# Kernel tuning notes

Hardware: AMD Instinct MI355X
Metric: run time of the kernel (lower is better)

Reference implementation:

```python
import jax, jax.numpy as jnp
import numpy as np

B, T, C = 8, 2048, 1024
H, K = 16, 31  # num_heads, kernel_size; head_size = C // H = 64


def setup_inputs() -> dict:
    key = jax.random.key(0)
    ks = jax.random.split(key, 3)
    x = jax.random.normal(ks[0], (B, T, C), dtype=jnp.float32)
    Wk = jax.random.normal(ks[1], (C, 2 * C), dtype=jnp.float32) * 0.02
    bk = jnp.zeros((2 * C,), dtype=jnp.float32)
    Wck = jax.random.normal(ks[2], (C, K * H), dtype=jnp.float32) * 0.02
    bck = jnp.zeros((K * H,), dtype=jnp.float32)
    gamma = jnp.ones((C,), dtype=jnp.float32)
    beta = jnp.zeros((C,), dtype=jnp.float32)
    conv_bias = jnp.zeros((C,), dtype=jnp.float32)
    return {"x": x, "Wk": Wk, "bk": bk, "Wck": Wck, "bck": bck,
            "gamma": gamma, "beta": beta, "conv_bias": conv_bias}


def _layernorm(x, g, b, eps=1e-5):
    mu = jnp.mean(x, axis=-1, keepdims=True)
    var = jnp.mean(jnp.square(x - mu), axis=-1, keepdims=True)
    return (x - mu) * jax.lax.rsqrt(var + eps) * g + b


def reference(x, Wk, bk, Wck, bck, gamma, beta, conv_bias):
    b, t, c = x.shape
    hd = c // H  # head size
    h = _layernorm(x, gamma, beta)
    pre = h @ Wk + bk                      # [B,T,2C]
    a, gte = jnp.split(pre, 2, axis=-1)
    k = a * jax.nn.sigmoid(gte)            # GLU -> [B,T,C]
    w = (k @ Wck + bck).reshape(b, t, H, K)
    w = jax.nn.softmax(w, axis=-1)         # per-token per-head kernel
    pad = K // 2
    kp = jnp.pad(k, ((0, 0), (pad, pad), (0, 0))).reshape(b, t + 2 * pad, H, hd)
    # depthwise dynamic conv: sum over K shifted slices (no im2col blowup)
    out = sum(w[:, :, :, i:i + 1] * kp[:, i:i + t] for i in range(K))  # [B,T,H,hd]
    out = out.reshape(b, t, c) + conv_bias + x  # bias + residual
    return out
```

## Files before the change

kernel.cpp:

```cpp
#include <hip/hip_runtime.h>


typedef __bf16 bf16_t;
typedef __attribute__((ext_vector_type(8))) __bf16 bf16x8;
typedef __attribute__((ext_vector_type(4))) __bf16 bf16x4;
typedef __attribute__((ext_vector_type(4))) float f32x4;

__device__ __forceinline__ void gload_lds16(const void* g, void* l) {
  void* gg = const_cast<void*>(g);
  __builtin_amdgcn_global_load_lds(
      (__attribute__((address_space(1))) unsigned int*)gg,
      (__attribute__((address_space(3))) unsigned int*)l, 16, 0, 0);
}

__global__ __launch_bounds__(256) void prep_wk(const float* __restrict__ Wk,
                                               bf16_t* __restrict__ WT) {
  __shared__ bf16_t T[64][66];
  int c0 = blockIdx.x * 64;
  int k0 = blockIdx.y * 64;
  int tid = threadIdx.x;
#pragma unroll
  for (int p = 0; p < 4; ++p) {
    int idx = p * 256 + tid;
    int r = idx >> 4;
    int q = idx & 15;
    int strip = q >> 3;
    int col4 = (q & 7) * 4;
    const float* src = Wk + (size_t)(k0 + r) * 2048 + strip * 1024 + (c0 >> 1) + col4;
    float4 v = *(const float4*)src;
#pragma unroll
    for (int j = 0; j < 4; ++j) {
      int cl = (col4 + j) * 2 + strip;
      T[cl][r] = (bf16_t)((&v.x)[j]);
    }
  }
  __syncthreads();
  int c = tid >> 2;
  int kk = (tid & 3) * 16;
#pragma unroll
  for (int u = 0; u < 2; ++u) {
    bf16x8 o;
#pragma unroll
    for (int j = 0; j < 8; ++j) o[j] = T[c][kk + u * 8 + j];
    *(bf16x8*)&WT[(size_t)(c0 + c) * 1024 + k0 + kk + u * 8] = o;
  }
}

__global__ __launch_bounds__(256) void prep_wck(const float* __restrict__ Wck,
                                                bf16_t* __restrict__ WT) {
  __shared__ bf16_t T[64][66];
  int n0 = blockIdx.x * 64;
  int k0 = blockIdx.y * 64;
  int tid = threadIdx.x;
#pragma unroll
  for (int p = 0; p < 4; ++p) {
    int idx = p * 256 + tid;
    int r = idx >> 4;
    int q = idx & 15;
    int col = n0 + q * 4;
    float4 v = {0.f, 0.f, 0.f, 0.f};
    if (col < 496) v = *(const float4*)(Wck + (size_t)(k0 + r) * 496 + col);
#pragma unroll
    for (int j = 0; j < 4; ++j) T[q * 4 + j][r] = (bf16_t)((&v.x)[j]);
  }
  __syncthreads();
  int c = tid >> 2;
  int kk = (tid & 3) * 16;
#pragma unroll
  for (int u = 0; u < 2; ++u) {
    bf16x8 o;
#pragma unroll
    for (int j = 0; j < 8; ++j) o[j] = T[c][kk + u * 8 + j];
    *(bf16x8*)&WT[(size_t)(n0 + c) * 1024 + k0 + kk + u * 8] = o;
  }
}

__global__ __launch_bounds__(256) void ln_kernel(const float* __restrict__ x,
                                                 const float* __restrict__ gamma,
                                                 const float* __restrict__ beta,
                                                 bf16_t* __restrict__ h) {
  int row = blockIdx.x;
  int tid = threadIdx.x;
  int lane = tid & 63, wid = tid >> 6;
  const float4* xr = (const float4*)(x + (size_t)row * 1024);
  float4 v = xr[tid];
  __shared__ float red[4];
  __shared__ float bc[2];
  float s = v.x + v.y + v.z + v.w;
#pragma unroll
  for (int off = 32; off > 0; off >>= 1) s += __shfl_down(s, off);
  if (lane == 0) red[wid] = s;
  __syncthreads();
  if (tid == 0) bc[0] = (red[0] + red[1] + red[2] + red[3]) * (1.f / 1024.f);
  __syncthreads();
  float mu = bc[0];
  float dx = v.x - mu, dy = v.y - mu, dz = v.z - mu, dw = v.w - mu;
  float s2 = dx * dx + dy * dy + dz * dz + dw * dw;
#pragma unroll
  for (int off = 32; off > 0; off >>= 1) s2 += __shfl_down(s2, off);
  if (lane == 0) red[wid] = s2;
  __syncthreads();
  if (tid == 0)
    bc[1] = rsqrtf((red[0] + red[1] + red[2] + red[3]) * (1.f / 1024.f) + 1e-5f);
  __syncthreads();
  float rs = bc[1];
  const float4* g4 = (const float4*)gamma;
  const float4* b4 = (const float4*)beta;
  float4 gv = g4[tid], bv = b4[tid];
  bf16x4 o;
  o[0] = (bf16_t)(dx * rs * gv.x + bv.x);
  o[1] = (bf16_t)(dy * rs * gv.y + bv.y);
  o[2] = (bf16_t)(dz * rs * gv.z + bv.z);
  o[3] = (bf16_t)(dw * rs * gv.w + bv.w);
  *(bf16x4*)&h[(size_t)row * 1024 + tid * 4] = o;
}

__global__ __launch_bounds__(512, 2) void gemm256_glu(const bf16_t* __restrict__ Ag,
                                                      const bf16_t* __restrict__ Bg,
                                                      const float* __restrict__ bias,
                                                      bf16_t* __restrict__ outp) {
  extern __shared__ char smem[];
  const int tid = threadIdx.x;
  const int lane = tid & 63;
  const int wid = tid >> 6;
  const int wr = wid >> 2;
  const int wc = wid & 3;

  int bid = blockIdx.x;
  int swz = (bid & 7) * 64 + (bid >> 3);
  int m0 = (swz >> 3) * 256;
  int n0 = (swz & 7) * 256;

  const int xr = (lane & 7) << 4;
  const int cs0 = (((lane >> 4) << 4) ^ xr);
  const int cs1 = cs0 ^ 64;
  const int aBase = wr * 16384 + (lane & 15) * 128;
  const int bBase = 65536 + (wc >> 1) * 16384 + (wc & 1) * 8192 + (lane & 15) * 128;

  const int sidx0 = tid, sidx1 = tid + 512;
  const int srow0 = sidx0 >> 3, srow1 = sidx1 >> 3;
  const int scol0 = ((((sidx0 & 7) << 4) ^ ((srow0 & 7) << 4)) >> 1);
  const int scol1 = ((((sidx1 & 7) << 4) ^ ((srow1 & 7) << 4)) >> 1);
  const int d0 = sidx0 * 16, d1 = sidx1 * 16;

  f32x4 acc[8][4] = {};
  bf16x8 bq[4][2], pc[2][2], pn[2][2];

#define STAGE_A(buf, h_, kt)                                                          \
  {                                                                                   \
    gload_lds16(Ag + (size_t)(m0 + (h_)*128 + srow0) * 1024 + (kt) + scol0,           \
                smem + (buf)*32768 + (h_)*16384 + d0);                                \
    gload_lds16(Ag + (size_t)(m0 + (h_)*128 + srow1) * 1024 + (kt) + scol1,           \
                smem + (buf)*32768 + (h_)*16384 + d1);                                \
  }
#define STAGE_B(buf, h_, kt)                                                          \
  {                                                                                   \
    gload_lds16(Bg + (size_t)(n0 + (h_)*128 + srow0) * 1024 + (kt) + scol0,           \
                smem + 65536 + (buf)*32768 + (h_)*16384 + d0);                        \
    gload_lds16(Bg + (size_t)(n0 + (h_)*128 + srow1) * 1024 + (kt) + scol1,           \
                smem + 65536 + (buf)*32768 + (h_)*16384 + d1);                        \
  }
#define LDA(buf, f, s) (*(const bf16x8*)(smem + (buf)*32768 + aBase + (f)*2048 + ((s) ? cs1 : cs0)))
#define LDB(buf, g, s) (*(const bf16x8*)(smem + bBase + (buf)*32768 + (g)*2048 + ((s) ? cs1 : cs0)))
#define MFMA_(a, b, c) __builtin_amdgcn_mfma_f32_16x16x32_bf16(a, b, c, 0, 0, 0)
#define RD_PAIR(D, buf, f)                                                            \
  { D[0][0] = LDA(buf, f, 0); D[0][1] = LDA(buf, f, 1);                               \
    D[1][0] = LDA(buf, (f) + 1, 0); D[1][1] = LDA(buf, (f) + 1, 1); }
#define RD_BQ(buf)                                                                    \
  { _Pragma("unroll") for (int g = 0; g < 4; ++g) {                                   \
      bq[g][0] = LDB(buf, g, 0); bq[g][1] = LDB(buf, g, 1); } }
#define MM_PAIR(F0, P)                                                                \
  { _Pragma("unroll") for (int g = 0; g < 4; ++g) {                                   \
      acc[F0][g]       = MFMA_(P[0][0], bq[g][0], acc[F0][g]);                        \
      acc[(F0) + 1][g] = MFMA_(P[1][0], bq[g][0], acc[(F0) + 1][g]);                  \
      acc[F0][g]       = MFMA_(P[0][1], bq[g][1], acc[F0][g]);                        \
      acc[(F0) + 1][g] = MFMA_(P[1][1], bq[g][1], acc[(F0) + 1][g]); } }
#define LGKM0                                                                         \
  asm volatile("s_waitcnt lgkmcnt(0)" ::: "memory");                                  \
  __builtin_amdgcn_sched_barrier(0)
#define BAR __builtin_amdgcn_s_barrier()
#define PRIO1 __builtin_amdgcn_s_setprio(1)
#define PRIO0 __builtin_amdgcn_s_setprio(0)

#define TILE(BUF, NBUF, T)                                                            \
  {                                                                                   \
                                                                              \
    BAR;                                                                              \
    if ((T) < 15) { STAGE_A(NBUF, 0, ((T) + 1) * 64); STAGE_A(NBUF, 1, ((T) + 1) * 64); } \
    LGKM0; PRIO1; MM_PAIR(0, pc); PRIO0;                                              \
    RD_PAIR(pn, BUF, 2);                                                              \
                                                                              \
    BAR;                                                                              \
    LGKM0; PRIO1; MM_PAIR(2, pn); PRIO0;                                              \
    RD_PAIR(pc, BUF, 4);                                                              \
                                                                              \
    BAR;                                                                              \
    if ((T) < 14) STAGE_B(BUF, 0, ((T) + 2) * 64);                                    \
    LGKM0; PRIO1; MM_PAIR(4, pc); PRIO0;                                              \
    RD_PAIR(pn, BUF, 6);                                                              \
                                                                              \
    if ((T) < 14)       { asm volatile("s_waitcnt vmcnt(2)" ::: "memory"); }          \
    else if ((T) == 14) { asm volatile("s_waitcnt vmcnt(0)" ::: "memory"); }          \
    BAR;                                                                              \
    if ((T) < 14) STAGE_B(BUF, 1, ((T) + 2) * 64);                                    \
    LGKM0; PRIO1; MM_PAIR(6, pn); PRIO0;                                              \
    if ((T) < 15) { RD_BQ(NBUF); RD_PAIR(pc, NBUF, 0); }                              \
  }

  STAGE_B(0, 0, 0); STAGE_B(0, 1, 0); STAGE_A(0, 0, 0); STAGE_A(0, 1, 0);
  STAGE_B(1, 0, 64); STAGE_B(1, 1, 64);
  asm volatile("s_waitcnt vmcnt(4)" ::: "memory");
  BAR;
  RD_BQ(0); RD_PAIR(pc, 0, 0);

  for (int t = 0; t < 14; t += 2) {
    TILE(0, 1, t);
    TILE(1, 0, t + 1);
  }
  TILE(0, 1, 14);
  TILE(1, 0, 15);

#pragma unroll
  for (int f = 0; f < 8; ++f) {
    int row = m0 + wr * 128 + f * 16 + ((lane >> 4) << 2);
#pragma unroll
    for (int g = 0; g < 4; ++g) {
      int col = n0 + wc * 64 + g * 16 + (lane & 15);
      int src = (col & 1) ? 1024 + (col >> 1) : (col >> 1);
      float bv = bias[src];
#pragma unroll
      for (int j = 0; j < 4; ++j) {
        float v = acc[f][g][j] + bv;
        float gt = __shfl_xor(v, 1);
        if (!(col & 1)) {
          float kv = v / (1.f + __expf(-gt));
          outp[(size_t)(row + j) * 1024 + (col >> 1)] = (bf16_t)kv;
        }
      }
    }
  }
#undef STAGE_A
#undef STAGE_B
#undef LDA
#undef LDB
#undef MFMA_
#undef RD_PAIR
#undef RD_BQ
#undef MM_PAIR
#undef LGKM0
#undef BAR
#undef PRIO1
#undef PRIO0
#undef TILE
}

__global__ __launch_bounds__(256, 2) void gemm128_bias(const bf16_t* __restrict__ Ag,
                                                       const bf16_t* __restrict__ Bg,
                                                       const float* __restrict__ bias,
                                                       float* __restrict__ outp) {
  __shared__ bf16_t As[2][128 * 32];
  __shared__ bf16_t Bs[2][128 * 32];
  int tid = threadIdx.x;
  int lane = tid & 63;
  int wid = tid >> 6;
  int wr = wid >> 1, wc = wid & 1;
  int n0 = blockIdx.x * 128;
  int m0 = blockIdx.y * 128;

  f32x4 acc[4][4] = {};

#define STAGE(bufi, kt)                                                         \
  {                                                                             \
    _Pragma("unroll") for (int s_ = 0; s_ < 2; ++s_) {                          \
      int idx = (tid + s_ * 256) * 8;                                           \
      int row = idx >> 5;                                                       \
      int col = idx & 31;                                                       \
      gload_lds16(Ag + (size_t)(m0 + row) * 1024 + (kt) + col, &As[bufi][idx]); \
      gload_lds16(Bg + (size_t)(n0 + row) * 1024 + (kt) + col, &Bs[bufi][idx]); \
    }                                                                           \
  }

#define COMPUTE(bufi)                                                           \
  {                                                                             \
    int ko = (lane >> 4) * 8;                                                   \
    int rl = lane & 15;                                                         \
    bf16x8 af[4], bb[4];                                                        \
    _Pragma("unroll") for (int m_ = 0; m_ < 4; ++m_)                            \
        af[m_] = *(const bf16x8*)&As[bufi][(wr * 64 + m_ * 16 + rl) * 32 + ko]; \
    _Pragma("unroll") for (int n_ = 0; n_ < 4; ++n_)                            \
        bb[n_] = *(const bf16x8*)&Bs[bufi][(wc * 64 + n_ * 16 + rl) * 32 + ko]; \
    _Pragma("unroll") for (int m_ = 0; m_ < 4; ++m_)                            \
        _Pragma("unroll") for (int n_ = 0; n_ < 4; ++n_)                        \
            acc[m_][n_] = __builtin_amdgcn_mfma_f32_16x16x32_bf16(              \
                af[m_], bb[n_], acc[m_][n_], 0, 0, 0);                          \
  }

  STAGE(0, 0);
  __syncthreads();
  int buf = 0;
  for (int kt = 32; kt < 1024; kt += 32) {
    STAGE(buf ^ 1, kt);
    COMPUTE(buf);
    __syncthreads();
    buf ^= 1;
  }
  COMPUTE(buf);

#pragma unroll
  for (int m_ = 0; m_ < 4; ++m_) {
    int row = m0 + wr * 64 + m_ * 16 + ((lane >> 4) << 2);
#pragma unroll
    for (int n_ = 0; n_ < 4; ++n_) {
      int col = n0 + wc * 64 + n_ * 16 + (lane & 15);
      float bv = (col < 496) ? bias[col] : 0.f;
#pragma unroll
      for (int j = 0; j < 4; ++j)
        outp[(size_t)(row + j) * 512 + col] = acc[m_][n_][j] + bv;
    }
  }
#undef STAGE
#undef COMPUTE
}

__global__ __launch_bounds__(256) void conv_kernel(const bf16_t* __restrict__ Kin,
                                                   const float* __restrict__ logits,
                                                   const float* __restrict__ x,
                                                   const float* __restrict__ conv_bias,
                                                   float* __restrict__ out) {
  __shared__ bf16_t ks[94][64];
  __shared__ float wls[64][32];
  int tid = threadIdx.x;
  int t0 = blockIdx.x * 64;
  int hh = blockIdx.y;
  int b = blockIdx.z;

  for (int i = tid; i < 94 * 8; i += 256) {
    int r = i >> 3;
    int seg = (i & 7) * 8;
    int t = t0 - 15 + r;
    bf16x8 v = {};
    if (t >= 0 && t < 2048)
      v = *(const bf16x8*)&Kin[((size_t)b * 2048 + t) * 1024 + hh * 64 + seg];
    *(bf16x8*)&ks[r][seg] = v;
  }
  if (tid < 64) {
    int t = t0 + tid;
    const float* lp = logits + ((size_t)b * 2048 + t) * 512 + hh * 31;
    float l[31];
    float mx = -1e30f;
#pragma unroll
    for (int i = 0; i < 31; ++i) { l[i] = lp[i]; mx = fmaxf(mx, l[i]); }
    float ssum = 0.f;
#pragma unroll
    for (int i = 0; i < 31; ++i) { l[i] = __expf(l[i] - mx); ssum += l[i]; }
    float inv = 1.f / ssum;
#pragma unroll
    for (int i = 0; i < 31; ++i) wls[tid][i] = l[i] * inv;
  }
  __syncthreads();

  int lane = tid & 63;
  int tq = tid >> 6;
  float win[46];
#pragma unroll
  for (int j = 0; j < 46; ++j) win[j] = (float)ks[tq * 16 + j][lane];
  float cb = conv_bias[hh * 64 + lane];
#pragma unroll
  for (int j = 0; j < 16; ++j) {
    int trow = tq * 16 + j;
    float wv[31];
#pragma unroll
    for (int i4 = 0; i4 < 7; ++i4) {
      f32x4 w4 = *(const f32x4*)&wls[trow][i4 * 4];
      wv[i4 * 4 + 0] = w4[0]; wv[i4 * 4 + 1] = w4[1];
      wv[i4 * 4 + 2] = w4[2]; wv[i4 * 4 + 3] = w4[3];
    }
    wv[28] = wls[trow][28]; wv[29] = wls[trow][29]; wv[30] = wls[trow][30];
    float a = 0.f;
#pragma unroll
    for (int i = 0; i < 31; ++i) a += wv[i] * win[j + i];
    size_t off = ((size_t)b * 2048 + t0 + trow) * 1024 + hh * 64 + lane;
    out[off] = a + cb + x[off];
  }
}

extern "C" void kernel_launch(void* const* d_in, const int* in_sizes, int n_in,
                              void* d_out, int out_size, void* d_ws, size_t ws_size,
                              hipStream_t stream) {
  const float* x         = (const float*)d_in[0];
  const float* Wk        = (const float*)d_in[1];
  const float* bk        = (const float*)d_in[2];
  const float* Wck       = (const float*)d_in[3];
  const float* bck       = (const float*)d_in[4];
  const float* gamma     = (const float*)d_in[5];
  const float* beta      = (const float*)d_in[6];
  const float* conv_bias = (const float*)d_in[7];
  float* out = (float*)d_out;

  char* ws = (char*)d_ws;
  bf16_t* h      = (bf16_t*)(ws);
  bf16_t* kbuf   = (bf16_t*)(ws + (33554432));
  bf16_t* WT1    = (bf16_t*)(ws + (67108864));
  bf16_t* WT2    = (bf16_t*)(ws + (71303168));
  float*  logits = (float*)(ws + (72351744));

  hipFuncSetAttribute((const void*)gemm256_glu,
                      hipFuncAttributeMaxDynamicSharedMemorySize, 131072);

  prep_wk<<<dim3(32, 16), 256, 0, stream>>>(Wk, WT1);
  prep_wck<<<dim3(8, 16), 256, 0, stream>>>(Wck, WT2);
  ln_kernel<<<16384, 256, 0, stream>>>(x, gamma, beta, h);
  gemm256_glu<<<512, 512, 131072, stream>>>(h, WT1, bk, kbuf);
  gemm128_bias<<<dim3(4, 128), 256, 0, stream>>>(kbuf, WT2, bck, logits);
  conv_kernel<<<dim3(32, 16, 8), 256, 0, stream>>>(kbuf, logits, x, conv_bias, out);
}
```

Before: 290.6 us.

## Fuse softmax into logits GEMM epilogue with head-padded layout, bf16 weights

Reorders the Wck columns so each head occupies 32 slots (31 taps plus one pad), which lets the second GEMM compute the per-head softmax in its epilogue through lane shuffles and store normalized weights as bf16. The conv kernel then reads the precomputed weights with vector loads instead of 64 threads doing a serial 31-wide softmax from fp32 logits. LayerNorm now handles one row per wavefront with shuffle-only reductions and no block barriers. The fused epilogue adds shuffle and exp work to the GEMM, and storing the weights in bf16 lowers their precision.

```diff
diff --git a/kernel.cpp b/kernel.cpp
--- a/kernel.cpp
+++ b/kernel.cpp
@@ -57,11 +57,15 @@
     int idx = p * 256 + tid;
     int r = idx >> 4;
     int q = idx & 15;
-    int col = n0 + q * 4;
-    float4 v = {0.f, 0.f, 0.f, 0.f};
-    if (col < 496) v = *(const float4*)(Wck + (size_t)(k0 + r) * 496 + col);
-#pragma unroll
-    for (int j = 0; j < 4; ++j) T[q * 4 + j][r] = (bf16_t)((&v.x)[j]);
+#pragma unroll
+    for (int j = 0; j < 4; ++j) {
+      int nl = q * 4 + j;
+      int n = n0 + nl;
+      int hh = n >> 5, kk = n & 31;
+      float val = 0.f;
+      if (kk < 31) val = Wck[(size_t)(k0 + r) * 496 + hh * 31 + kk];
+      T[nl][r] = (bf16_t)val;
+    }
   }
   __syncthreads();
   int c = tid >> 2;
@@ -79,40 +83,39 @@
                                                  const float* __restrict__ gamma,
                                                  const float* __restrict__ beta,
                                                  bf16_t* __restrict__ h) {
-  int row = blockIdx.x;
   int tid = threadIdx.x;
-  int lane = tid & 63, wid = tid >> 6;
-  const float4* xr = (const float4*)(x + (size_t)row * 1024);
-  float4 v = xr[tid];
-  __shared__ float red[4];
-  __shared__ float bc[2];
-  float s = v.x + v.y + v.z + v.w;
-#pragma unroll
-  for (int off = 32; off > 0; off >>= 1) s += __shfl_down(s, off);
-  if (lane == 0) red[wid] = s;
-  __syncthreads();
-  if (tid == 0) bc[0] = (red[0] + red[1] + red[2] + red[3]) * (1.f / 1024.f);
-  __syncthreads();
-  float mu = bc[0];
-  float dx = v.x - mu, dy = v.y - mu, dz = v.z - mu, dw = v.w - mu;
-  float s2 = dx * dx + dy * dy + dz * dz + dw * dw;
-#pragma unroll
-  for (int off = 32; off > 0; off >>= 1) s2 += __shfl_down(s2, off);
-  if (lane == 0) red[wid] = s2;
-  __syncthreads();
-  if (tid == 0)
-    bc[1] = rsqrtf((red[0] + red[1] + red[2] + red[3]) * (1.f / 1024.f) + 1e-5f);
-  __syncthreads();
-  float rs = bc[1];
-  const float4* g4 = (const float4*)gamma;
-  const float4* b4 = (const float4*)beta;
-  float4 gv = g4[tid], bv = b4[tid];
-  bf16x4 o;
-  o[0] = (bf16_t)(dx * rs * gv.x + bv.x);
-  o[1] = (bf16_t)(dy * rs * gv.y + bv.y);
-  o[2] = (bf16_t)(dz * rs * gv.z + bv.z);
-  o[3] = (bf16_t)(dw * rs * gv.w + bv.w);
-  *(bf16x4*)&h[(size_t)row * 1024 + tid * 4] = o;
+  int lane = tid & 63;
+  int row = blockIdx.x * 4 + (tid >> 6);
+  const float* xr = x + (size_t)row * 1024;
+  float4 v[4];
+#pragma unroll
+  for (int u = 0; u < 4; ++u) v[u] = *(const float4*)(xr + u * 256 + lane * 4);
+  float s = 0.f;
+#pragma unroll
+  for (int u = 0; u < 4; ++u) s += v[u].x + v[u].y + v[u].z + v[u].w;
+#pragma unroll
+  for (int off = 32; off > 0; off >>= 1) s += __shfl_xor(s, off);
+  float mu = s * (1.f / 1024.f);
+  float s2 = 0.f;
+#pragma unroll
+  for (int u = 0; u < 4; ++u) {
+    float a = v[u].x - mu, b = v[u].y - mu, c = v[u].z - mu, d = v[u].w - mu;
+    s2 += a * a + b * b + c * c + d * d;
+  }
+#pragma unroll
+  for (int off = 32; off > 0; off >>= 1) s2 += __shfl_xor(s2, off);
+  float rs = rsqrtf(s2 * (1.f / 1024.f) + 1e-5f);
+#pragma unroll
+  for (int u = 0; u < 4; ++u) {
+    float4 gv = *(const float4*)(gamma + u * 256 + lane * 4);
+    float4 bv = *(const float4*)(beta + u * 256 + lane * 4);
+    bf16x4 o;
+    o[0] = (bf16_t)((v[u].x - mu) * rs * gv.x + bv.x);
+    o[1] = (bf16_t)((v[u].y - mu) * rs * gv.y + bv.y);
+    o[2] = (bf16_t)((v[u].z - mu) * rs * gv.z + bv.z);
+    o[3] = (bf16_t)((v[u].w - mu) * rs * gv.w + bv.w);
+    *(bf16x4*)&h[(size_t)row * 1024 + u * 256 + lane * 4] = o;
+  }
 }
 
 __global__ __launch_bounds__(512, 2) void gemm256_glu(const bf16_t* __restrict__ Ag,
@@ -254,10 +257,10 @@
 #undef TILE
 }
 
-__global__ __launch_bounds__(256, 2) void gemm128_bias(const bf16_t* __restrict__ Ag,
-                                                       const bf16_t* __restrict__ Bg,
-                                                       const float* __restrict__ bias,
-                                                       float* __restrict__ outp) {
+__global__ __launch_bounds__(256, 2) void gemm128_sm(const bf16_t* __restrict__ Ag,
+                                                     const bf16_t* __restrict__ Bg,
+                                                     const float* __restrict__ bck,
+                                                     bf16_t* __restrict__ Wout) {
   __shared__ bf16_t As[2][128 * 32];
   __shared__ bf16_t Bs[2][128 * 32];
   int tid = threadIdx.x;
@@ -306,16 +309,37 @@
   }
   COMPUTE(buf);
 
+  int s = lane & 15;
+  int slotB = s + 16;
 #pragma unroll
   for (int m_ = 0; m_ < 4; ++m_) {
     int row = m0 + wr * 64 + m_ * 16 + ((lane >> 4) << 2);
 #pragma unroll
-    for (int n_ = 0; n_ < 4; ++n_) {
-      int col = n0 + wc * 64 + n_ * 16 + (lane & 15);
-      float bv = (col < 496) ? bias[col] : 0.f;
-#pragma unroll
-      for (int j = 0; j < 4; ++j)
-        outp[(size_t)(row + j) * 512 + col] = acc[m_][n_][j] + bv;
+    for (int pp = 0; pp < 2; ++pp) {
+      int colA = n0 + wc * 64 + pp * 32 + s;
+      int hh = colA >> 5;
+      float bvA = bck[hh * 31 + s];
+      float bvB = (slotB < 31) ? bck[hh * 31 + slotB] : 0.f;
+#pragma unroll
+      for (int j = 0; j < 4; ++j) {
+        float v0 = acc[m_][2 * pp][j] + bvA;
+        float v1 = (slotB < 31) ? (acc[m_][2 * pp + 1][j] + bvB) : -1e30f;
+        float mx = fmaxf(v0, v1);
+        mx = fmaxf(mx, __shfl_xor(mx, 1));
+        mx = fmaxf(mx, __shfl_xor(mx, 2));
+        mx = fmaxf(mx, __shfl_xor(mx, 4));
+        mx = fmaxf(mx, __shfl_xor(mx, 8));
+        float e0 = __expf(v0 - mx);
+        float e1 = (slotB < 31) ? __expf(v1 - mx) : 0.f;
+        float ss = e0 + e1;
+        ss += __shfl_xor(ss, 1);
+        ss += __shfl_xor(ss, 2);
+        ss += __shfl_xor(ss, 4);
+        ss += __shfl_xor(ss, 8);
+        float inv = 1.f / ss;
+        Wout[(size_t)(row + j) * 512 + colA] = (bf16_t)(e0 * inv);
+        Wout[(size_t)(row + j) * 512 + colA + 16] = (bf16_t)(e1 * inv);
+      }
     }
   }
 #undef STAGE
@@ -323,7 +347,7 @@
 }
 
 __global__ __launch_bounds__(256) void conv_kernel(const bf16_t* __restrict__ Kin,
-                                                   const float* __restrict__ logits,
+                                                   const bf16_t* __restrict__ Wq,
                                                    const float* __restrict__ x,
                                                    const float* __restrict__ conv_bias,
                                                    float* __restrict__ out) {
@@ -343,19 +367,11 @@
       v = *(const bf16x8*)&Kin[((size_t)b * 2048 + t) * 1024 + hh * 64 + seg];
     *(bf16x8*)&ks[r][seg] = v;
   }
-  if (tid < 64) {
-    int t = t0 + tid;
-    const float* lp = logits + ((size_t)b * 2048 + t) * 512 + hh * 31;
-    float l[31];
-    float mx = -1e30f;
-#pragma unroll
-    for (int i = 0; i < 31; ++i) { l[i] = lp[i]; mx = fmaxf(mx, l[i]); }
-    float ssum = 0.f;
-#pragma unroll
-    for (int i = 0; i < 31; ++i) { l[i] = __expf(l[i] - mx); ssum += l[i]; }
-    float inv = 1.f / ssum;
-#pragma unroll
-    for (int i = 0; i < 31; ++i) wls[tid][i] = l[i] * inv;
+  {
+    int tok = tid >> 2, part = tid & 3;
+    bf16x8 wv8 = *(const bf16x8*)&Wq[((size_t)b * 2048 + t0 + tok) * 512 + hh * 32 + part * 8];
+#pragma unroll
+    for (int j = 0; j < 8; ++j) wls[tok][part * 8 + j] = (float)wv8[j];
   }
   __syncthreads();
 
@@ -402,15 +418,15 @@
   bf16_t* kbuf   = (bf16_t*)(ws + (33554432));
   bf16_t* WT1    = (bf16_t*)(ws + (67108864));
   bf16_t* WT2    = (bf16_t*)(ws + (71303168));
-  float*  logits = (float*)(ws + (72351744));
+  bf16_t* Wq     = (bf16_t*)(ws + (72351744));
 
   hipFuncSetAttribute((const void*)gemm256_glu,
                       hipFuncAttributeMaxDynamicSharedMemorySize, 131072);
 
   prep_wk<<<dim3(32, 16), 256, 0, stream>>>(Wk, WT1);
   prep_wck<<<dim3(8, 16), 256, 0, stream>>>(Wck, WT2);
-  ln_kernel<<<16384, 256, 0, stream>>>(x, gamma, beta, h);
+  ln_kernel<<<4096, 256, 0, stream>>>(x, gamma, beta, h);
   gemm256_glu<<<512, 512, 131072, stream>>>(h, WT1, bk, kbuf);
-  gemm128_bias<<<dim3(4, 128), 256, 0, stream>>>(kbuf, WT2, bck, logits);
-  conv_kernel<<<dim3(32, 16, 8), 256, 0, stream>>>(kbuf, logits, x, conv_bias, out);
-}
+  gemm128_sm<<<dim3(4, 128), 256, 0, stream>>>(kbuf, WT2, bck, Wq);
+  conv_kernel<<<dim3(32, 16, 8), 256, 0, stream>>>(kbuf, Wq, x, conv_bias, out);
+}
```

After: 289.0 us. About the same (-0.5%).
